# Optimization experiments

Hardware: AMD Instinct MI355X
Metric: run time of the kernel (lower is better)

## Reference

```python
import jax, jax.numpy as jnp
import numpy as np

B, O, K, GS = 4096, 11008, 4096, 128  # batch, out_features, in_features, group_size
G = K // GS  # num groups = 32


def _unpack_int4(packed):
    """packed: [N, K//2] int values in [0,256) holding two 4-bit nibbles (low first).
    Returns signed int4 values as float32 [N, K]."""
    low = packed & 15
    high = (packed >> 4) & 15
    q = jnp.stack([low, high], axis=-1).reshape(packed.shape[0], -1)  # interleave low,high
    return jnp.where(q >= 8, q - 16, q).astype(jnp.float32)


def setup_inputs() -> dict:
    key = jax.random.key(0)
    k1, k2, k3, k4, k5 = jax.random.split(key, 5)
    x = jax.random.randint(k1, (B, K // 2), 0, 256, dtype=jnp.int32)
    a_scale = jax.random.uniform(k2, (B, G), dtype=jnp.float32).astype(jnp.float16)
    w_packed = jax.random.randint(k3, (O, K // 2), 0, 256, dtype=jnp.int32)
    w_scale = jax.random.uniform(k4, (O, G), dtype=jnp.float32).astype(jnp.float16)
    bias = (jax.random.normal(k5, (O,), dtype=jnp.float32) * 0.02).astype(jnp.float16)
    return {"x": x, "a_scale": a_scale, "w_packed": w_packed, "w_scale": w_scale,
            "bias": bias, "group_size": GS}


def reference(x, a_scale, w_packed, w_scale, bias, group_size):
    # out[b,o] = sum_g a_scale[b,g] * w_scale[o,g] * sum_{k in g} x_int4[b,k] * w_int4[o,k] + bias[o]
    # Fold the per-group scales into the dequantized operands, then a single GEMM
    # (mathematically identical to group-wise int accumulate + dequant).
    b, o = x.shape[0], w_packed.shape[0]
    k = x.shape[1] * 2
    g = k // group_size
    xq = _unpack_int4(x).reshape(b, g, group_size) * a_scale.astype(jnp.float32)[:, :, None]
    wq = _unpack_int4(w_packed).reshape(o, g, group_size) * w_scale.astype(jnp.float32)[:, :, None]
    out = jnp.einsum('bgk,ogk->bo', xq, wq).astype(jnp.float16)  # [B, O] fp16
    return out + bias
```

## Files before the change

### kernel.cpp

```cpp
#include <hip/hip_runtime.h>


#define B_DIM 4096
#define O_DIM 11008
#define K_DIM 4096
#define G_NUM 32

#define NX32 8388608u
#define NW32 22544384u
#define X8_BYTES  16777216u
#define W8_BYTES  45088768u

typedef int   i32x4 __attribute__((ext_vector_type(4)));
typedef float f32x4 __attribute__((ext_vector_type(4)));

__device__ __forceinline__ unsigned pack2(int v) {
    int t = v ^ 0x88;
    unsigned lo = (unsigned)(((t & 15) - 8) & 0xFF);
    unsigned hi = (unsigned)((((t >> 4) & 15) - 8) & 0xFF);
    return lo | (hi << 8);
}

__global__ __launch_bounds__(256)
void unpack_kernel(const int* __restrict__ xq, const int* __restrict__ wq,
                   unsigned char* __restrict__ X8, unsigned char* __restrict__ W8) {
    unsigned t = blockIdx.x * 256u + threadIdx.x;
    const int* src;
    unsigned char* dst;
    if (t < NX32 / 8) {
        src = xq + (size_t)t * 8;
        dst = X8 + (size_t)t * 16;
    } else {
        unsigned j = t - NX32 / 8;
        src = wq + (size_t)j * 8;
        dst = W8 + (size_t)j * 16;
    }
    int4 v0 = ((const int4*)src)[0];
    int4 v1 = ((const int4*)src)[1];
    uint4 o;
    o.x = pack2(v0.x) | (pack2(v0.y) << 16);
    o.y = pack2(v0.z) | (pack2(v0.w) << 16);
    o.z = pack2(v1.x) | (pack2(v1.y) << 16);
    o.w = pack2(v1.z) | (pack2(v1.w) << 16);
    *(uint4*)dst = o;
}

__global__ __launch_bounds__(256)
void tscale_kernel(const float* __restrict__ as_, const float* __restrict__ ws_,
                   float* __restrict__ asT, float* __restrict__ wsT) {
    __shared__ float tile[64][33];
    const int blk = blockIdx.x, t = threadIdx.x;
    const float* src; float* dst; int R0, RTOT;
    if (blk < 64) { src = as_; dst = asT; R0 = blk * 64;        RTOT = B_DIM; }
    else          { src = ws_; dst = wsT; R0 = (blk - 64) * 64; RTOT = O_DIM; }

    {
        const int r = t >> 2, cc = (t & 3) * 8;
        const float* p = src + (size_t)(R0 + r) * G_NUM + cc;
        f32x4 v0 = *(const f32x4*)p;
        f32x4 v1 = *(const f32x4*)(p + 4);
#pragma unroll
        for (int k = 0; k < 4; ++k) { tile[r][cc + k] = v0[k]; tile[r][cc + 4 + k] = v1[k]; }
    }
    __syncthreads();
    {
        const int g = t >> 3, bc = (t & 7) * 8;
        f32x4 w0, w1;
#pragma unroll
        for (int k = 0; k < 4; ++k) { w0[k] = tile[bc + k][g]; w1[k] = tile[bc + 4 + k][g]; }
        float* q = dst + (size_t)g * RTOT + R0 + bc;
        *(f32x4*)q = w0;
        *(f32x4*)(q + 4) = w1;
    }
}

__global__ __launch_bounds__(256, 2)
void gemm_i8(const unsigned char* __restrict__ X8, const unsigned char* __restrict__ W8,
             const float* __restrict__ asT, const float* __restrict__ wsT,
             const float* __restrict__ bias, float* __restrict__ out) {
    __shared__ __align__(16) unsigned char A0[16384];
    __shared__ __align__(16) unsigned char B0[16384];
    __shared__ __align__(16) unsigned char A1[16384];
    __shared__ __align__(16) unsigned char B1[16384];

    const int tid  = threadIdx.x;
    const int wv   = tid >> 6;
    const int lane = tid & 63;
    const int quad = lane >> 4;
    const int lq   = lane & 15;

    const unsigned lin = blockIdx.x;
    const unsigned xcd = lin & 7u, pos = lin >> 3;
    const int bn = (int)(pos % 86u);
    const int bm = (int)((xcd << 2) + pos / 86u);

    const int wm   = (wv & 1) << 6;
    const int wn   = (wv >> 1) << 6;

    f32x4 facc[4][4] = {};

    const int l8 = lane >> 3;
    const int c8 = lane & 7;
    const int sw_chunk = ((c8 ^ l8) << 4);
    const size_t xrow0 = (size_t)(bm * 128) * K_DIM;
    const size_t wrow0 = (size_t)(bn * 128) * K_DIM;
    const int abase = bm * 128 + wm + (quad << 2);
    const int wbase = bn * 128 + wn + lq;
    const int pa0 = ((quad ^ (lq & 7)) << 4);
    const int pa1 = (((4 + quad) ^ (lq & 7)) << 4);

    auto stageA = [&](int g, unsigned char* Ad) {
        const int gb = g << 7;
#pragma unroll
        for (int s = 0; s < 4; ++s) {
            const int slab = (wv << 2) + s;
            const int row  = (slab << 3) + l8;
            const unsigned char* gp = X8 + xrow0 + (size_t)row * K_DIM + gb + sw_chunk;
            __builtin_amdgcn_global_load_lds(
                (const __attribute__((address_space(1))) void*)gp,
                (__attribute__((address_space(3))) void*)(Ad + (slab << 10)), 16, 0, 0);
        }
    };
    auto stageB = [&](int g, unsigned char* Bd) {
        const int gb = g << 7;
#pragma unroll
        for (int s = 0; s < 4; ++s) {
            const int slab = (wv << 2) + s;
            const int row  = (slab << 3) + l8;
            const unsigned char* gp = W8 + wrow0 + (size_t)row * K_DIM + gb + sw_chunk;
            __builtin_amdgcn_global_load_lds(
                (const __attribute__((address_space(1))) void*)gp,
                (__attribute__((address_space(3))) void*)(Bd + (slab << 10)), 16, 0, 0);
        }
    };
    auto loadScales = [&](int g, f32x4 (&asr)[4], float (&wsn)[4]) {
#pragma unroll
        for (int i = 0; i < 4; ++i)
            asr[i] = *(const f32x4*)&asT[(g << 12) + abase + (i << 4)];
#pragma unroll
        for (int j = 0; j < 4; ++j)
            wsn[j] = wsT[(size_t)g * O_DIM + wbase + (j << 4)];
    };

    f32x4 asrA[4], asrB[4];
    float wsnA[4], wsnB[4];

    auto body = [&](int g, const unsigned char* Ac, const unsigned char* Bc,
                    unsigned char* An, unsigned char* Bn,
                    f32x4 (&asrC)[4], float (&wsnC)[4],
                    f32x4 (&asrN)[4], float (&wsnN)[4]) {
        const int gn = (g + 1 < G_NUM) ? g + 1 : G_NUM - 1;
        i32x4 gacc[4][4] = {};
        i32x4 av0[4], bv0[4], av1[4], bv1[4];

#pragma unroll
        for (int i = 0; i < 4; ++i)
            av0[i] = *(const i32x4*)&Ac[((wm + (i << 4) + lq) << 7) + pa0];
        stageA(gn, An);
        asm volatile("s_waitcnt vmcnt(12)" ::: "memory");
        __builtin_amdgcn_s_barrier();
        __builtin_amdgcn_sched_barrier(0);

#pragma unroll
        for (int j = 0; j < 4; ++j)
            bv0[j] = *(const i32x4*)&Bc[((wn + (j << 4) + lq) << 7) + pa0];
        stageB(gn, Bn);
        asm volatile("s_waitcnt lgkmcnt(0)" ::: "memory");
        __builtin_amdgcn_sched_barrier(0);
        __builtin_amdgcn_s_setprio(1);
#pragma unroll
        for (int i = 0; i < 4; ++i)
#pragma unroll
            for (int j = 0; j < 4; ++j)
                gacc[i][j] = __builtin_amdgcn_mfma_i32_16x16x64_i8(av0[i], bv0[j], gacc[i][j], 0, 0, 0);
        __builtin_amdgcn_s_setprio(0);

#pragma unroll
        for (int i = 0; i < 4; ++i)
            av1[i] = *(const i32x4*)&Ac[((wm + (i << 4) + lq) << 7) + pa1];
#pragma unroll
        for (int j = 0; j < 4; ++j)
            bv1[j] = *(const i32x4*)&Bc[((wn + (j << 4) + lq) << 7) + pa1];
        loadScales(gn, asrN, wsnN);
        asm volatile("s_waitcnt lgkmcnt(0)" ::: "memory");
        __builtin_amdgcn_sched_barrier(0);
        __builtin_amdgcn_s_setprio(1);
#pragma unroll
        for (int i = 0; i < 4; ++i)
#pragma unroll
            for (int j = 0; j < 4; ++j)
                gacc[i][j] = __builtin_amdgcn_mfma_i32_16x16x64_i8(av1[i], bv1[j], gacc[i][j], 0, 0, 0);
        __builtin_amdgcn_s_setprio(0);

        asm volatile("s_waitcnt vmcnt(16)" ::: "memory");
        __builtin_amdgcn_sched_barrier(0);
#pragma unroll
        for (int i = 0; i < 4; ++i)
#pragma unroll
            for (int j = 0; j < 4; ++j) {
                f32x4 s = asrC[i] * wsnC[j];
                f32x4 gf;
#pragma unroll
                for (int r = 0; r < 4; ++r) gf[r] = (float)gacc[i][j][r];
                facc[i][j] += gf * s;
            }
        asm volatile("s_waitcnt vmcnt(12)" ::: "memory");
        __builtin_amdgcn_s_barrier();
        __builtin_amdgcn_sched_barrier(0);
    };

    stageA(0, A0);
    stageB(0, B0);
    loadScales(0, asrA, wsnA);
    asm volatile("s_waitcnt vmcnt(12)" ::: "memory");
    __builtin_amdgcn_s_barrier();
    __builtin_amdgcn_sched_barrier(0);

#pragma unroll 1
    for (int g2 = 0; g2 < G_NUM; g2 += 2) {
        body(g2,     A0, B0, A1, B1, asrA, wsnA, asrB, wsnB);
        body(g2 + 1, A1, B1, A0, B0, asrB, wsnB, asrA, wsnA);
    }

    const int n0 = bn * 128 + wn + lq;
    const int m0 = bm * 128 + wm + (quad << 2);
    float bvs[4];
#pragma unroll
    for (int j = 0; j < 4; ++j) bvs[j] = bias[n0 + (j << 4)];
#pragma unroll
    for (int i = 0; i < 4; ++i) {
#pragma unroll
        for (int r = 0; r < 4; ++r) {
            float* orow = out + (size_t)(m0 + (i << 4) + r) * O_DIM;
#pragma unroll
            for (int j = 0; j < 4; ++j)
                orow[n0 + (j << 4)] = facc[i][j][r] + bvs[j];
        }
    }
}

extern "C" void kernel_launch(void* const* d_in, const int* in_sizes, int n_in,
                              void* d_out, int out_size, void* d_ws, size_t ws_size,
                              hipStream_t stream) {
    const int*   xq   = (const int*)d_in[0];
    const float* as_  = (const float*)d_in[1];
    const int*   wq   = (const int*)d_in[2];
    const float* ws_  = (const float*)d_in[3];
    const float* bias = (const float*)d_in[4];
    float* out        = (float*)d_out;

    unsigned char* X8 = (unsigned char*)d_ws;
    unsigned char* W8 = X8 + X8_BYTES;
    float* asT = (float*)((unsigned char*)d_ws + X8_BYTES + W8_BYTES);
    float* wsT = asT + (size_t)G_NUM * B_DIM;

    unpack_kernel<<<(NX32 + NW32) / 8 / 256, 256, 0, stream>>>(xq, wq, X8, W8);
    tscale_kernel<<<64 + 172, 256, 0, stream>>>(as_, ws_, asT, wsT);
    gemm_i8<<<dim3((B_DIM / 128) * (O_DIM / 128)), 256, 0, stream>>>(X8, W8, asT, wsT, bias, out);
}
```

Baseline: 561.4 us.

## Merge A/B staging behind one barrier per group and drop XCD block swizzle

Each K-group iteration now has a single barrier at its top, after waiting for the previous stage's LDS loads. A and B tiles are prefetched together right after the first-half fragment reads, and the scale loads for the next group are issued at the end of the body. The launch changes from a 1D grid with an XCD-aware tile remap to a plain 2D grid indexed by bm/bn. The aim is to cut barrier overhead and simplify the vmcnt schedule, but losing the remap may reduce L2 reuse across the chiplets.

```diff
diff --git a/kernel.cpp b/kernel.cpp
--- a/kernel.cpp
+++ b/kernel.cpp
@@ -53,7 +53,6 @@
     const float* src; float* dst; int R0, RTOT;
     if (blk < 64) { src = as_; dst = asT; R0 = blk * 64;        RTOT = B_DIM; }
     else          { src = ws_; dst = wsT; R0 = (blk - 64) * 64; RTOT = O_DIM; }
-
     {
         const int r = t >> 2, cc = (t & 3) * 8;
         const float* p = src + (size_t)(R0 + r) * G_NUM + cc;
@@ -88,12 +87,8 @@
     const int lane = tid & 63;
     const int quad = lane >> 4;
     const int lq   = lane & 15;
-
-    const unsigned lin = blockIdx.x;
-    const unsigned xcd = lin & 7u, pos = lin >> 3;
-    const int bn = (int)(pos % 86u);
-    const int bm = (int)((xcd << 2) + pos / 86u);
-
+    const int bm   = blockIdx.x;
+    const int bn   = blockIdx.y;
     const int wm   = (wv & 1) << 6;
     const int wn   = (wv >> 1) << 6;
 
@@ -109,27 +104,24 @@
     const int pa0 = ((quad ^ (lq & 7)) << 4);
     const int pa1 = (((4 + quad) ^ (lq & 7)) << 4);
 
-    auto stageA = [&](int g, unsigned char* Ad) {
+    auto stageAB = [&](int g, unsigned char* Ad, unsigned char* Bd) {
         const int gb = g << 7;
 #pragma unroll
         for (int s = 0; s < 4; ++s) {
             const int slab = (wv << 2) + s;
             const int row  = (slab << 3) + l8;
-            const unsigned char* gp = X8 + xrow0 + (size_t)row * K_DIM + gb + sw_chunk;
+            const unsigned char* gpA = X8 + xrow0 + (size_t)row * K_DIM + gb + sw_chunk;
             __builtin_amdgcn_global_load_lds(
-                (const __attribute__((address_space(1))) void*)gp,
+                (const __attribute__((address_space(1))) void*)gpA,
                 (__attribute__((address_space(3))) void*)(Ad + (slab << 10)), 16, 0, 0);
         }
-    };
-    auto stageB = [&](int g, unsigned char* Bd) {
-        const int gb = g << 7;
 #pragma unroll
         for (int s = 0; s < 4; ++s) {
             const int slab = (wv << 2) + s;
             const int row  = (slab << 3) + l8;
-            const unsigned char* gp = W8 + wrow0 + (size_t)row * K_DIM + gb + sw_chunk;
+            const unsigned char* gpB = W8 + wrow0 + (size_t)row * K_DIM + gb + sw_chunk;
             __builtin_amdgcn_global_load_lds(
-                (const __attribute__((address_space(1))) void*)gp,
+                (const __attribute__((address_space(1))) void*)gpB,
                 (__attribute__((address_space(3))) void*)(Bd + (slab << 10)), 16, 0, 0);
         }
     };
@@ -153,18 +145,18 @@
         i32x4 gacc[4][4] = {};
         i32x4 av0[4], bv0[4], av1[4], bv1[4];
 
+        asm volatile("s_waitcnt vmcnt(8)" ::: "memory");
+        __builtin_amdgcn_s_barrier();
+        __builtin_amdgcn_sched_barrier(0);
+
 #pragma unroll
         for (int i = 0; i < 4; ++i)
             av0[i] = *(const i32x4*)&Ac[((wm + (i << 4) + lq) << 7) + pa0];
-        stageA(gn, An);
-        asm volatile("s_waitcnt vmcnt(12)" ::: "memory");
-        __builtin_amdgcn_s_barrier();
-        __builtin_amdgcn_sched_barrier(0);
-
 #pragma unroll
         for (int j = 0; j < 4; ++j)
             bv0[j] = *(const i32x4*)&Bc[((wn + (j << 4) + lq) << 7) + pa0];
-        stageB(gn, Bn);
+        stageAB(gn, An, Bn);
+
         asm volatile("s_waitcnt lgkmcnt(0)" ::: "memory");
         __builtin_amdgcn_sched_barrier(0);
         __builtin_amdgcn_s_setprio(1);
@@ -181,7 +173,6 @@
 #pragma unroll
         for (int j = 0; j < 4; ++j)
             bv1[j] = *(const i32x4*)&Bc[((wn + (j << 4) + lq) << 7) + pa1];
-        loadScales(gn, asrN, wsnN);
         asm volatile("s_waitcnt lgkmcnt(0)" ::: "memory");
         __builtin_amdgcn_sched_barrier(0);
         __builtin_amdgcn_s_setprio(1);
@@ -192,7 +183,7 @@
                 gacc[i][j] = __builtin_amdgcn_mfma_i32_16x16x64_i8(av1[i], bv1[j], gacc[i][j], 0, 0, 0);
         __builtin_amdgcn_s_setprio(0);
 
-        asm volatile("s_waitcnt vmcnt(16)" ::: "memory");
+        asm volatile("s_waitcnt vmcnt(8)" ::: "memory");
         __builtin_amdgcn_sched_barrier(0);
 #pragma unroll
         for (int i = 0; i < 4; ++i)
@@ -204,17 +195,11 @@
                 for (int r = 0; r < 4; ++r) gf[r] = (float)gacc[i][j][r];
                 facc[i][j] += gf * s;
             }
-        asm volatile("s_waitcnt vmcnt(12)" ::: "memory");
-        __builtin_amdgcn_s_barrier();
-        __builtin_amdgcn_sched_barrier(0);
+        loadScales(gn, asrN, wsnN);
     };
 
-    stageA(0, A0);
-    stageB(0, B0);
+    stageAB(0, A0, B0);
     loadScales(0, asrA, wsnA);
-    asm volatile("s_waitcnt vmcnt(12)" ::: "memory");
-    __builtin_amdgcn_s_barrier();
-    __builtin_amdgcn_sched_barrier(0);
 
 #pragma unroll 1
     for (int g2 = 0; g2 < G_NUM; g2 += 2) {
@@ -256,5 +241,5 @@
 
     unpack_kernel<<<(NX32 + NW32) / 8 / 256, 256, 0, stream>>>(xq, wq, X8, W8);
     tscale_kernel<<<64 + 172, 256, 0, stream>>>(as_, ws_, asT, wsT);
-    gemm_i8<<<dim3((B_DIM / 128) * (O_DIM / 128)), 256, 0, stream>>>(X8, W8, asT, wsT, bias, out);
-}
+    gemm_i8<<<dim3(B_DIM / 128, O_DIM / 128), 256, 0, stream>>>(X8, W8, asT, wsT, bias, out);
+}
```

Measured after the change: 544.9 us. -3.0%, faster.
